# Optimization experiments

Hardware: AMD Instinct MI355X
Metric: run time of the kernel (lower is better)

## Reference

```python
import jax, jax.numpy as jnp
import numpy as np

# H2RConfig constants
KERNEL = 3
MAX_ROUTES = 1000
STRIDE = 4.0
MIN_SIZE = 32.0
MAX_SIZE = 512.0
SCORE_POWER = 2.0
UNC_WEIGHT = 0.35


def setup_inputs() -> dict:
    key = jax.random.key(0)
    k1, k2, k3 = jax.random.split(key, 3)
    shape = (32, 1, 512, 512)  # [B, 1, H, W] heatmaps at stride 4
    return {
        "route_logits": jax.random.normal(k1, shape, jnp.float32),
        "scale_logits": jax.random.normal(k2, shape, jnp.float32),
        "uncertainty_logits": jax.random.normal(k3, shape, jnp.float32),
        "image_h": 2048,
        "image_w": 2048,
    }


def reference(route_logits, scale_logits, uncertainty_logits, image_h, image_w):
    # score map: sigmoid^power, modulated by uncertainty (use_route_uncertainty=True)
    score = jnp.power(jax.nn.sigmoid(route_logits), SCORE_POWER)
    score = score * (1.0 - UNC_WEIGHT * jax.nn.sigmoid(uncertainty_logits))

    # local-max NMS: 3x3 max pool, stride 1, SAME padding (torch pads with -inf)
    pooled = jax.lax.reduce_window(
        score, -jnp.inf, jax.lax.max,
        window_dimensions=(1, 1, KERNEL, KERNEL),
        window_strides=(1, 1, 1, 1),
        padding="SAME",
    )
    peak_mask = score == pooled
    filtered = jnp.where(peak_mask, score, -1.0)

    B = score.shape[0]
    Wd = score.shape[3]
    flat = filtered.reshape(B, -1)                 # [B, H*W]
    values, indices = jax.lax.top_k(flat, MAX_ROUTES)  # [B, K]
    valid = values > 0.0                            # torch drops these; we mask/pad

    ys = indices // Wd
    xs = indices % Wd
    cx = (xs.astype(jnp.float32) + 0.5) * STRIDE
    cy = (ys.astype(jnp.float32) + 0.5) * STRIDE

    # gather scale / uncertainty at peak locations
    sc = jnp.take_along_axis(scale_logits.reshape(B, -1), indices, axis=1)
    un = jax.nn.sigmoid(jnp.take_along_axis(uncertainty_logits.reshape(B, -1), indices, axis=1))

    side = MIN_SIZE + jax.nn.sigmoid(sc) * (MAX_SIZE - MIN_SIZE)
    side = side * (1.0 + 0.25 * un)
    half = side * 0.5

    iw = float(image_w)
    ih = float(image_h)
    x1 = jnp.clip(cx - half, 0.0, iw - 1.0)
    y1 = jnp.clip(cy - half, 0.0, ih - 1.0)
    x2 = jnp.clip(cx + half, 1.0, iw)
    y2 = jnp.clip(cy + half, 1.0, ih)

    bcol = jnp.broadcast_to(jnp.arange(B, dtype=jnp.float32)[:, None], values.shape)
    rois = jnp.stack([bcol, x1, y1, x2, y2], axis=-1)  # [B, K, 5]

    # padded (fixed-shape) equivalent of torch's variable-length concat
    rois = jnp.where(valid[..., None], rois, 0.0)
    scores = jnp.where(valid, values, 0.0)
    return rois, scores, valid
```

## Files before the change

kernel.cpp:

```cpp
#include <hip/hip_runtime.h>
#include <hip/hip_bf16.h>
#include <math.h>


#define B_   32
#define H_   512
#define W_   512
#define HW_  (H_ * W_)
#define K_   1000
#define ROWS_ 16
#define THR_  512
#define NSTRIP_ 32
#define SEGCAP_ 1200
#define CAND_ 2048
#define NBUK_ 4096
#define NW_   (NBUK_ / 2)

__device__ __forceinline__ float np_expf(float x) {
#pragma clang fp contract(off)
    const float log2e = 1.44269504088896341f;
    float z = x * log2e;
    float m = rintf(z);
    float r = fmaf(m, -0.693359375f, x);
    r = fmaf(m, 2.12194440e-4f, r);
    float r2 = r * r;
    float p = fmaf(1.9875691500e-4f, r, 1.3981999507e-3f);
    p = fmaf(p, r, 8.3334519073e-3f);
    p = fmaf(p, r, 4.1665795894e-2f);
    p = fmaf(p, r, 1.6666665459e-1f);
    p = fmaf(p, r, 5.0000001201e-1f);
    p = fmaf(p, r2, r);
    p = p + 1.0f;
    int mi = (int)m;
    float sc = __int_as_float((127 + mi) << 23);
    return p * sc;
}

__device__ __forceinline__ float sigmoid_np(float x) {
#pragma clang fp contract(off)
    float e = np_expf(-x);
    float d = 1.0f + e;
    return 1.0f / d;
}

__device__ __forceinline__ float score_ref(float r, float u) {
#pragma clang fp contract(off)
    float s  = sigmoid_np(r);
    float s2 = s * s;
    float su = sigmoid_np(u);
    float t  = 0.35f * su;
    float m  = 1.0f - t;
    return s2 * m;
}

__device__ __forceinline__ float sigmoid_fast(float x) {
    return 1.0f / (1.0f + __expf(-x));
}

__global__ __launch_bounds__(THR_, 4) void fused_peak_kernel(
    const float* __restrict__ route, const float* __restrict__ unc,
    unsigned long long* __restrict__ plist, int* __restrict__ pcnt)
{
    __shared__ float sm[ROWS_ + 2][W_];
    __shared__ int lcnt;

    const int tid   = threadIdx.x;
    const int lane  = tid & 63;
    const int strip = blockIdx.x;
    const int b     = blockIdx.y;
    const int r0    = strip * ROWS_;
    if (tid == 0) lcnt = 0;

    const float4* rb4 = (const float4*)(route + (size_t)b * HW_);
    const float4* ub4 = (const float4*)(unc   + (size_t)b * HW_);
    unsigned long long* seg =
        plist + (size_t)(b * NSTRIP_ + strip) * SEGCAP_;

    float4 rv[5], uv[5];
    int lrow[5], c4[5]; bool ok[5];
    #pragma unroll
    for (int k = 0; k < 5; ++k) {
        int slot = tid + k * THR_;
        slot = slot < 2303 ? slot : 2303;
        int row = slot >> 7;
        int gy  = r0 - 1 + row;
        lrow[k] = row; c4[k] = slot & 127;
        ok[k]   = (gy >= 0 && gy < H_);
        int cy  = gy < 0 ? 0 : (gy >= H_ ? H_ - 1 : gy);
        rv[k] = rb4[cy * 128 + c4[k]];
        uv[k] = ub4[cy * 128 + c4[k]];
    }
    #pragma unroll
    for (int k = 0; k < 5; ++k) {
        float4 s;
        s.x = score_ref(rv[k].x, uv[k].x);
        s.y = score_ref(rv[k].y, uv[k].y);
        s.z = score_ref(rv[k].z, uv[k].z);
        s.w = score_ref(rv[k].w, uv[k].w);
        if (!ok[k]) { s.x = -INFINITY; s.y = -INFINITY;
                      s.z = -INFINITY; s.w = -INFINITY; }
        *(float4*)&sm[lrow[k]][c4[k] * 4] = s;
    }
    __syncthreads();

    #pragma unroll
    for (int j = 0; j < 4; ++j) {
        int g  = tid + j * THR_;
        int ly = 1 + (g >> 7);
        int x0 = (g & 127) * 4;
        int gy = r0 + (ly - 1);
        float4 q0 = *(const float4*)&sm[ly - 1][x0];
        float4 q1 = *(const float4*)&sm[ly    ][x0];
        float4 q2 = *(const float4*)&sm[ly + 1][x0];
        bool hasL = (x0 > 0), hasR = (x0 + 4 < W_);
        float l0 = hasL ? sm[ly - 1][x0 - 1] : -INFINITY;
        float l1 = hasL ? sm[ly    ][x0 - 1] : -INFINITY;
        float l2 = hasL ? sm[ly + 1][x0 - 1] : -INFINITY;
        float e0 = hasR ? sm[ly - 1][x0 + 4] : -INFINITY;
        float e1 = hasR ? sm[ly    ][x0 + 4] : -INFINITY;
        float e2 = hasR ? sm[ly + 1][x0 + 4] : -INFINITY;
        float f_m1 = fmaxf(l0, fmaxf(l1, l2));
        float f_0  = fmaxf(q0.x, fmaxf(q1.x, q2.x));
        float f_1  = fmaxf(q0.y, fmaxf(q1.y, q2.y));
        float f_2  = fmaxf(q0.z, fmaxf(q1.z, q2.z));
        float f_3  = fmaxf(q0.w, fmaxf(q1.w, q2.w));
        float f_4  = fmaxf(e0, fmaxf(e1, e2));
        float tb0  = fmaxf(q0.x, q2.x);
        float tb1  = fmaxf(q0.y, q2.y);
        float tb2  = fmaxf(q0.z, q2.z);
        float tb3  = fmaxf(q0.w, q2.w);
        float vv[4] = { q1.x, q1.y, q1.z, q1.w };
        float mm[4];
        mm[0] = fmaxf(fmaxf(f_m1, f_1), tb0);
        mm[1] = fmaxf(fmaxf(f_0,  f_2), tb1);
        mm[2] = fmaxf(fmaxf(f_1,  f_3), tb2);
        mm[3] = fmaxf(fmaxf(f_2,  f_4), tb3);
        #pragma unroll
        for (int i = 0; i < 4; ++i) {
            bool take = (vv[i] >= mm[i]);
            unsigned long long mk = __ballot(take);
            if (mk) {
                int ldr = __ffsll((unsigned long long)mk) - 1;
                int base_ = 0;
                if (lane == ldr) base_ = atomicAdd(&lcnt, __popcll(mk));
                base_ = __shfl(base_, ldr, 64);
                if (take) {
                    int p = base_ + __popcll(mk & ((1ull << lane) - 1ull));
                    unsigned int bits = __float_as_uint(vv[i]);
                    unsigned int idx  = (unsigned int)(gy * W_ + x0 + i);
                    if (p < SEGCAP_)
                        seg[p] = ((unsigned long long)bits << 32)
                                 | (0xFFFFFFFFu - idx);
                }
            }
        }
    }
    __syncthreads();
    if (tid == 0) {
        int n = lcnt < SEGCAP_ ? lcnt : SEGCAP_;
        pcnt[b * NSTRIP_ + strip] = n;
    }
}

__global__ __launch_bounds__(1024) void select_kernel(
    const float* __restrict__ scale, const float* __restrict__ unc,
    const unsigned long long* __restrict__ plist,
    const int* __restrict__ pcnt,
    const int* __restrict__ ih_p, const int* __restrict__ iw_p,
    float* __restrict__ out)
{
    __shared__ unsigned int h16[NW_];
    __shared__ unsigned long long cand[CAND_];
    __shared__ int scnt[NSTRIP_];
    __shared__ int sh_T, sh_n;

    const int b = blockIdx.x, tid = threadIdx.x;
    const int lane = tid & 63, wid = tid >> 6;
    if (tid == 0) { sh_T = 0; sh_n = 0; }
    if (tid < NSTRIP_) scnt[tid] = pcnt[b * NSTRIP_ + tid];
    for (int i = tid; i < NW_; i += 1024) h16[i] = 0u;
    __syncthreads();

    for (int s = 0; s < NSTRIP_; ++s) {
        int cnt = scnt[s];
        const unsigned long long* sg =
            plist + (size_t)(b * NSTRIP_ + s) * SEGCAP_;
        for (int i = tid; i < cnt; i += 1024) {
            unsigned int bkt = ((unsigned int)(sg[i] >> 32)) >> 18;
            atomicAdd(&h16[bkt >> 1], 1u << ((bkt & 1) * 16));
        }
    }
    __syncthreads();

    if (wid == 0) {
        int total = 0;
        for (int c = NBUK_ / 64 - 1; c >= 0; --c) {
            int bucket = c * 64 + lane;
            int cnt = (int)((h16[bucket >> 1] >> ((bucket & 1) * 16)) & 0xFFFFu);
            int sum = cnt;
            #pragma unroll
            for (int off = 32; off > 0; off >>= 1)
                sum += __shfl_down(sum, off, 64);
            sum = __shfl(sum, 0, 64);
            if (total + sum < K_) { total += sum; continue; }
            int suf = cnt;
            #pragma unroll
            for (int off = 1; off < 64; off <<= 1) {
                int o = __shfl_down(suf, off, 64);
                suf += (lane + off < 64) ? o : 0;
            }
            bool cond = (total + suf) >= K_;
            unsigned long long mask = __ballot(cond);
            int ls = 63 - __builtin_clzll(mask);
            if (lane == 0) sh_T = c * 64 + ls;
            break;
        }
    }
    __syncthreads();
    const unsigned int T = (unsigned int)sh_T;

    for (int s = 0; s < NSTRIP_; ++s) {
        int cnt = scnt[s];
        const unsigned long long* sg =
            plist + (size_t)(b * NSTRIP_ + s) * SEGCAP_;
        for (int i = tid; i < cnt; i += 1024) {
            unsigned long long key = sg[i];
            if (((((unsigned int)(key >> 32))) >> 18) >= T) {
                int p = atomicAdd(&sh_n, 1);
                if (p < CAND_) cand[p] = key;
            }
        }
    }
    __syncthreads();
    int nc = sh_n; if (nc > CAND_) nc = CAND_;
    int sortN = (nc <= 1024) ? 1024 : CAND_;
    for (int i = tid; i < sortN; i += 1024)
        if (i >= nc) cand[i] = 0ull;

    for (int kk = 2; kk <= sortN; kk <<= 1) {
        for (int jj = kk >> 1; jj > 0; jj >>= 1) {
            __syncthreads();
            for (int p = tid; p < (sortN >> 1); p += 1024) {
                int i   = ((p & ~(jj - 1)) << 1) | (p & (jj - 1));
                int ixj = i | jj;
                bool desc = ((i & kk) == 0);
                unsigned long long a = cand[i], c2 = cand[ixj];
                if (desc ? (a < c2) : (a > c2)) { cand[i] = c2; cand[ixj] = a; }
            }
        }
    }
    __syncthreads();

    const float fih = (float)(*ih_p);
    const float fiw = (float)(*iw_p);
    float* rois   = out;
    float* scores = out + (size_t)B_ * K_ * 5;
    float* validf = out + (size_t)B_ * K_ * 6;

    for (int k = tid; k < K_; k += 1024) {
        int o = b * K_ + k;
        unsigned long long key = cand[k];
        unsigned int bits = (unsigned int)(key >> 32);
        if (bits == 0u) {
            rois[o * 5 + 0] = 0.0f; rois[o * 5 + 1] = 0.0f;
            rois[o * 5 + 2] = 0.0f; rois[o * 5 + 3] = 0.0f;
            rois[o * 5 + 4] = 0.0f;
            scores[o] = 0.0f; validf[o] = 0.0f;
        } else {
            float v = __uint_as_float(bits);
            unsigned int idx = 0xFFFFFFFFu - (unsigned int)(key & 0xFFFFFFFFull);
            int y = (int)(idx >> 9), x = (int)(idx & 511u);
            float cx = ((float)x + 0.5f) * 4.0f;
            float cy = ((float)y + 0.5f) * 4.0f;
            float ss = sigmoid_fast(scale[(size_t)b * HW_ + idx]);
            float su = sigmoid_fast(unc  [(size_t)b * HW_ + idx]);
            float side = (32.0f + ss * 480.0f) * (1.0f + 0.25f * su);
            float half = 0.5f * side;
            float x1 = fminf(fmaxf(cx - half, 0.0f), fiw - 1.0f);
            float y1 = fminf(fmaxf(cy - half, 0.0f), fih - 1.0f);
            float x2 = fminf(fmaxf(cx + half, 1.0f), fiw);
            float y2 = fminf(fmaxf(cy + half, 1.0f), fih);
            rois[o * 5 + 0] = (float)b;
            rois[o * 5 + 1] = x1; rois[o * 5 + 2] = y1;
            rois[o * 5 + 3] = x2; rois[o * 5 + 4] = y2;
            scores[o] = v; validf[o] = 1.0f;
        }
    }
}

extern "C" void kernel_launch(void* const* d_in, const int* in_sizes, int n_in,
                              void* d_out, int out_size, void* d_ws, size_t ws_size,
                              hipStream_t stream) {
    const float* route = (const float*)d_in[0];
    const float* scale = (const float*)d_in[1];
    const float* unc   = (const float*)d_in[2];
    const int*   ih    = (const int*)d_in[3];
    const int*   iw    = (const int*)d_in[4];
    float* out = (float*)d_out;

    char* ws = (char*)d_ws;
    int* pcnt = (int*)ws;
    unsigned long long* plist = (unsigned long long*)(ws + 4096);

    dim3 g(NSTRIP_, B_);
    fused_peak_kernel<<<g, THR_, 0, stream>>>(route, unc, plist, pcnt);
    select_kernel<<<B_, 1024, 0, stream>>>(scale, unc, plist, pcnt,
                                           ih, iw, out);
}
```

Before: 174.5 us.

## Zero-pad peak segments and scan them with wide loads, sharded histograms, warp-aggregated appends

The peak kernel now zero-fills the unused tail of each strip segment instead of writing per-strip counts. The select kernel can then stream the whole per-batch slot array with 16-byte loads, unrolled two pairs deep, with no per-strip loop or count lookups. The histogram is split into four shared-memory copies to reduce atomic contention, and the candidate append uses one wave-aggregated atomic per ballot. In exchange, every padded slot is read (about 38K keys per batch, regardless of the real count) and the peak kernel spends extra stores writing zeros.

```diff
diff --git a/kernel.cpp b/kernel.cpp
--- a/kernel.cpp
+++ b/kernel.cpp
@@ -12,6 +12,8 @@
 #define THR_  512
 #define NSTRIP_ 32
 #define SEGCAP_ 1200
+#define NSLOT_ (NSTRIP_ * SEGCAP_)
+#define NPAIR_ (NSLOT_ / 2)
 #define CAND_ 2048
 #define NBUK_ 4096
 #define NW_   (NBUK_ / 2)
@@ -59,7 +61,7 @@
 
 __global__ __launch_bounds__(THR_, 4) void fused_peak_kernel(
     const float* __restrict__ route, const float* __restrict__ unc,
-    unsigned long long* __restrict__ plist, int* __restrict__ pcnt)
+    unsigned long long* __restrict__ plist)
 {
     __shared__ float sm[ROWS_ + 2][W_];
     __shared__ int lcnt;
@@ -156,47 +158,62 @@
         }
     }
     __syncthreads();
-    if (tid == 0) {
-        int n = lcnt < SEGCAP_ ? lcnt : SEGCAP_;
-        pcnt[b * NSTRIP_ + strip] = n;
-    }
+    int n = lcnt < SEGCAP_ ? lcnt : SEGCAP_;
+    for (int i = n + tid; i < SEGCAP_; i += THR_) seg[i] = 0ull;
 }
 
 __global__ __launch_bounds__(1024) void select_kernel(
     const float* __restrict__ scale, const float* __restrict__ unc,
     const unsigned long long* __restrict__ plist,
-    const int* __restrict__ pcnt,
     const int* __restrict__ ih_p, const int* __restrict__ iw_p,
     float* __restrict__ out)
 {
-    __shared__ unsigned int h16[NW_];
+    __shared__ unsigned int h4[4 * NW_];
     __shared__ unsigned long long cand[CAND_];
-    __shared__ int scnt[NSTRIP_];
     __shared__ int sh_T, sh_n;
 
     const int b = blockIdx.x, tid = threadIdx.x;
     const int lane = tid & 63, wid = tid >> 6;
     if (tid == 0) { sh_T = 0; sh_n = 0; }
-    if (tid < NSTRIP_) scnt[tid] = pcnt[b * NSTRIP_ + tid];
-    for (int i = tid; i < NW_; i += 1024) h16[i] = 0u;
-    __syncthreads();
-
-    for (int s = 0; s < NSTRIP_; ++s) {
-        int cnt = scnt[s];
-        const unsigned long long* sg =
-            plist + (size_t)(b * NSTRIP_ + s) * SEGCAP_;
-        for (int i = tid; i < cnt; i += 1024) {
-            unsigned int bkt = ((unsigned int)(sg[i] >> 32)) >> 18;
-            atomicAdd(&h16[bkt >> 1], 1u << ((bkt & 1) * 16));
-        }
-    }
+    for (int i = tid; i < 4 * NW_; i += 1024) h4[i] = 0u;
+    __syncthreads();
+
+    const ulonglong2* p2 =
+        (const ulonglong2*)(plist + (size_t)b * NSLOT_);
+    unsigned int* hw = h4 + (wid >> 2) * NW_;
+
+    {
+        int i = tid;
+        for (; i + 1024 < NPAIR_; i += 2048) {
+            ulonglong2 a = p2[i];
+            ulonglong2 c = p2[i + 1024];
+            unsigned int b0 = ((unsigned int)(a.x >> 32)) >> 18;
+            unsigned int b1 = ((unsigned int)(a.y >> 32)) >> 18;
+            unsigned int b2 = ((unsigned int)(c.x >> 32)) >> 18;
+            unsigned int b3 = ((unsigned int)(c.y >> 32)) >> 18;
+            if (b0) atomicAdd(&hw[b0 >> 1], 1u << ((b0 & 1) * 16));
+            if (b1) atomicAdd(&hw[b1 >> 1], 1u << ((b1 & 1) * 16));
+            if (b2) atomicAdd(&hw[b2 >> 1], 1u << ((b2 & 1) * 16));
+            if (b3) atomicAdd(&hw[b3 >> 1], 1u << ((b3 & 1) * 16));
+        }
+        for (; i < NPAIR_; i += 1024) {
+            ulonglong2 a = p2[i];
+            unsigned int b0 = ((unsigned int)(a.x >> 32)) >> 18;
+            unsigned int b1 = ((unsigned int)(a.y >> 32)) >> 18;
+            if (b0) atomicAdd(&hw[b0 >> 1], 1u << ((b0 & 1) * 16));
+            if (b1) atomicAdd(&hw[b1 >> 1], 1u << ((b1 & 1) * 16));
+        }
+    }
+    __syncthreads();
+    for (int i = tid; i < NW_; i += 1024)
+        h4[i] = h4[i] + h4[NW_ + i] + h4[2 * NW_ + i] + h4[3 * NW_ + i];
     __syncthreads();
 
     if (wid == 0) {
         int total = 0;
         for (int c = NBUK_ / 64 - 1; c >= 0; --c) {
             int bucket = c * 64 + lane;
-            int cnt = (int)((h16[bucket >> 1] >> ((bucket & 1) * 16)) & 0xFFFFu);
+            int cnt = (int)((h4[bucket >> 1] >> ((bucket & 1) * 16)) & 0xFFFFu);
             int sum = cnt;
             #pragma unroll
             for (int off = 32; off > 0; off >>= 1)
@@ -219,15 +236,45 @@
     __syncthreads();
     const unsigned int T = (unsigned int)sh_T;
 
-    for (int s = 0; s < NSTRIP_; ++s) {
-        int cnt = scnt[s];
-        const unsigned long long* sg =
-            plist + (size_t)(b * NSTRIP_ + s) * SEGCAP_;
-        for (int i = tid; i < cnt; i += 1024) {
-            unsigned long long key = sg[i];
-            if (((((unsigned int)(key >> 32))) >> 18) >= T) {
-                int p = atomicAdd(&sh_n, 1);
-                if (p < CAND_) cand[p] = key;
+    {
+        int i = tid;
+        for (; i + 1024 < NPAIR_; i += 2048) {
+            ulonglong2 a = p2[i];
+            ulonglong2 c = p2[i + 1024];
+            unsigned long long ks[4] = { a.x, a.y, c.x, c.y };
+            #pragma unroll
+            for (int q = 0; q < 4; ++q) {
+                bool take = ((((unsigned int)(ks[q] >> 32))) >> 18) >= T;
+                unsigned long long mk = __ballot(take);
+                if (mk) {
+                    int ldr = __ffsll((unsigned long long)mk) - 1;
+                    int base_ = 0;
+                    if (lane == ldr) base_ = atomicAdd(&sh_n, __popcll(mk));
+                    base_ = __shfl(base_, ldr, 64);
+                    if (take) {
+                        int p = base_ + __popcll(mk & ((1ull << lane) - 1ull));
+                        if (p < CAND_) cand[p] = ks[q];
+                    }
+                }
+            }
+        }
+        for (; i < NPAIR_; i += 1024) {
+            ulonglong2 a = p2[i];
+            unsigned long long ks[2] = { a.x, a.y };
+            #pragma unroll
+            for (int q = 0; q < 2; ++q) {
+                bool take = ((((unsigned int)(ks[q] >> 32))) >> 18) >= T;
+                unsigned long long mk = __ballot(take);
+                if (mk) {
+                    int ldr = __ffsll((unsigned long long)mk) - 1;
+                    int base_ = 0;
+                    if (lane == ldr) base_ = atomicAdd(&sh_n, __popcll(mk));
+                    base_ = __shfl(base_, ldr, 64);
+                    if (take) {
+                        int p = base_ + __popcll(mk & ((1ull << lane) - 1ull));
+                        if (p < CAND_) cand[p] = ks[q];
+                    }
+                }
             }
         }
     }
@@ -298,12 +345,9 @@
     const int*   iw    = (const int*)d_in[4];
     float* out = (float*)d_out;
 
-    char* ws = (char*)d_ws;
-    int* pcnt = (int*)ws;
-    unsigned long long* plist = (unsigned long long*)(ws + 4096);
+    unsigned long long* plist = (unsigned long long*)d_ws;
 
     dim3 g(NSTRIP_, B_);
-    fused_peak_kernel<<<g, THR_, 0, stream>>>(route, unc, plist, pcnt);
-    select_kernel<<<B_, 1024, 0, stream>>>(scale, unc, plist, pcnt,
-                                           ih, iw, out);
-}
+    fused_peak_kernel<<<g, THR_, 0, stream>>>(route, unc, plist);
+    select_kernel<<<B_, 1024, 0, stream>>>(scale, unc, plist, ih, iw, out);
+}
```

Result: faster. 163.4 us (-6.4%).

## Pre-bucket peaks by score class per strip to skip select-kernel histogram pass

Applied to the files above, without the earlier changes.

The peak kernel now stages peaks in shared memory, builds a 512-class histogram over the score's float-bit exponent and mantissa bits, and writes each strip's peaks to global memory grouped by class, with the per-class counts emitted as 16-bit values. The select kernel sums these per-strip histograms to find the threshold class, then copies whole class-prefix ranges straight into the candidate buffer. This removes the select kernel's global histogram atomics and its filtered compaction pass. In exchange it adds shared-memory use and extra passes in the peak kernel, which may lower occupancy, and the candidate set (up to 4096) can be coarser, giving a larger bitonic sort.

```diff
diff --git a/kernel.cpp b/kernel.cpp
--- a/kernel.cpp
+++ b/kernel.cpp
@@ -12,9 +12,13 @@
 #define THR_  512
 #define NSTRIP_ 32
 #define SEGCAP_ 1200
-#define CAND_ 2048
-#define NBUK_ 4096
-#define NW_   (NBUK_ / 2)
+#define NCLS_ 512
+#define CAND4_ 4096
+
+__device__ __forceinline__ int class_of(unsigned int bits) {
+    int cls = 2031 - (int)(bits >> 19);
+    return cls > (NCLS_ - 1) ? (NCLS_ - 1) : cls;
+}
 
 __device__ __forceinline__ float np_expf(float x) {
 #pragma clang fp contract(off)
@@ -59,17 +63,22 @@
 
 __global__ __launch_bounds__(THR_, 4) void fused_peak_kernel(
     const float* __restrict__ route, const float* __restrict__ unc,
-    unsigned long long* __restrict__ plist, int* __restrict__ pcnt)
+    unsigned long long* __restrict__ plist, unsigned short* __restrict__ cnt16)
 {
     __shared__ float sm[ROWS_ + 2][W_];
+    __shared__ unsigned long long pbuf[SEGCAP_];
+    __shared__ unsigned int ccnt[NCLS_];
+    __shared__ unsigned int coff[NCLS_];
     __shared__ int lcnt;
 
     const int tid   = threadIdx.x;
     const int lane  = tid & 63;
+    const int wid   = tid >> 6;
     const int strip = blockIdx.x;
     const int b     = blockIdx.y;
     const int r0    = strip * ROWS_;
     if (tid == 0) lcnt = 0;
+    if (tid < NCLS_) ccnt[tid] = 0u;
 
     const float4* rb4 = (const float4*)(route + (size_t)b * HW_);
     const float4* ub4 = (const float4*)(unc   + (size_t)b * HW_);
@@ -149,93 +158,132 @@
                     unsigned int bits = __float_as_uint(vv[i]);
                     unsigned int idx  = (unsigned int)(gy * W_ + x0 + i);
                     if (p < SEGCAP_)
-                        seg[p] = ((unsigned long long)bits << 32)
-                                 | (0xFFFFFFFFu - idx);
+                        pbuf[p] = ((unsigned long long)bits << 32)
+                                  | (0xFFFFFFFFu - idx);
                 }
             }
         }
     }
     __syncthreads();
-    if (tid == 0) {
-        int n = lcnt < SEGCAP_ ? lcnt : SEGCAP_;
-        pcnt[b * NSTRIP_ + strip] = n;
-    }
+    const int n = lcnt < SEGCAP_ ? lcnt : SEGCAP_;
+
+    for (int i = tid; i < n; i += THR_)
+        atomicAdd(&ccnt[class_of((unsigned int)(pbuf[i] >> 32))], 1u);
+    __syncthreads();
+
+    if (wid == 0) {
+        int carry = 0;
+        for (int k = 0; k < NCLS_ / 64; ++k) {
+            int c = k * 64 + lane;
+            int v = (int)ccnt[c];
+            int pre = v;
+            #pragma unroll
+            for (int off = 1; off < 64; off <<= 1) {
+                int o = __shfl_up(pre, off, 64);
+                if (lane >= off) pre += o;
+            }
+            coff[c] = (unsigned int)(carry + pre - v);
+            carry += __shfl(pre, 63, 64);
+        }
+    }
+    __syncthreads();
+
+    for (int i = tid; i < n; i += THR_) {
+        unsigned long long key = pbuf[i];
+        int cls = class_of((unsigned int)(key >> 32));
+        unsigned int pos = atomicAdd(&coff[cls], 1u);
+        seg[pos] = key;
+    }
+    if (tid < NCLS_)
+        cnt16[(size_t)(b * NSTRIP_ + strip) * NCLS_ + tid] =
+            (unsigned short)ccnt[tid];
 }
 
 __global__ __launch_bounds__(1024) void select_kernel(
     const float* __restrict__ scale, const float* __restrict__ unc,
     const unsigned long long* __restrict__ plist,
-    const int* __restrict__ pcnt,
+    const unsigned short* __restrict__ cnt16,
     const int* __restrict__ ih_p, const int* __restrict__ iw_p,
     float* __restrict__ out)
 {
-    __shared__ unsigned int h16[NW_];
-    __shared__ unsigned long long cand[CAND_];
-    __shared__ int scnt[NSTRIP_];
-    __shared__ int sh_T, sh_n;
+    __shared__ __align__(16) unsigned char smem[CAND4_ * 8];
+    __shared__ unsigned int tot[NCLS_];
+    __shared__ int slen[NSTRIP_], sbase[NSTRIP_];
+    __shared__ int sh_C, sh_n;
+
+    unsigned int* scnt = (unsigned int*)smem;
+    unsigned long long* cand = (unsigned long long*)smem;
 
     const int b = blockIdx.x, tid = threadIdx.x;
     const int lane = tid & 63, wid = tid >> 6;
-    if (tid == 0) { sh_T = 0; sh_n = 0; }
-    if (tid < NSTRIP_) scnt[tid] = pcnt[b * NSTRIP_ + tid];
-    for (int i = tid; i < NW_; i += 1024) h16[i] = 0u;
-    __syncthreads();
-
+    if (tid == 0) { sh_C = NCLS_ - 1; sh_n = 0; }
+
+    const unsigned int* g =
+        (const unsigned int*)(cnt16 + (size_t)b * NSTRIP_ * NCLS_);
+    for (int i = tid; i < NSTRIP_ * NCLS_ / 2; i += 1024) scnt[i] = g[i];
+    __syncthreads();
+
+    if (tid < NCLS_) {
+        unsigned int s = 0;
+        for (int st = 0; st < NSTRIP_; ++st) {
+            unsigned int w = scnt[st * (NCLS_ / 2) + (tid >> 1)];
+            s += (tid & 1) ? (w >> 16) : (w & 0xFFFFu);
+        }
+        tot[tid] = s;
+    }
+    __syncthreads();
+
+    if (wid == 0) {
+        int cum = 0;
+        for (int k = 0; k < NCLS_ / 64; ++k) {
+            int c = k * 64 + lane;
+            int v = (int)tot[c];
+            int pre = v;
+            #pragma unroll
+            for (int off = 1; off < 64; off <<= 1) {
+                int o = __shfl_up(pre, off, 64);
+                if (lane >= off) pre += o;
+            }
+            int ctot = __shfl(pre, 63, 64);
+            if (cum + ctot < K_) { cum += ctot; continue; }
+            bool cond = (cum + pre) >= K_;
+            unsigned long long mask = __ballot(cond);
+            int fs = __ffsll((unsigned long long)mask) - 1;
+            if (lane == 0) sh_C = k * 64 + fs;
+            break;
+        }
+    }
+    __syncthreads();
+    const int Cstar = sh_C;
+
+    if (tid < NSTRIP_) {
+        int len = 0;
+        for (int c = 0; c <= Cstar; ++c) {
+            unsigned int w = scnt[tid * (NCLS_ / 2) + (c >> 1)];
+            len += (c & 1) ? (int)(w >> 16) : (int)(w & 0xFFFFu);
+        }
+        slen[tid] = len;
+    }
+    __syncthreads();
+    if (tid == 0) {
+        int acc = 0;
+        for (int s = 0; s < NSTRIP_; ++s) { sbase[s] = acc; acc += slen[s]; }
+        sh_n = acc;
+    }
+    __syncthreads();
+
+    const int n = sh_n < CAND4_ ? sh_n : CAND4_;
     for (int s = 0; s < NSTRIP_; ++s) {
-        int cnt = scnt[s];
+        int len = slen[s], base = sbase[s];
         const unsigned long long* sg =
             plist + (size_t)(b * NSTRIP_ + s) * SEGCAP_;
-        for (int i = tid; i < cnt; i += 1024) {
-            unsigned int bkt = ((unsigned int)(sg[i] >> 32)) >> 18;
-            atomicAdd(&h16[bkt >> 1], 1u << ((bkt & 1) * 16));
-        }
-    }
-    __syncthreads();
-
-    if (wid == 0) {
-        int total = 0;
-        for (int c = NBUK_ / 64 - 1; c >= 0; --c) {
-            int bucket = c * 64 + lane;
-            int cnt = (int)((h16[bucket >> 1] >> ((bucket & 1) * 16)) & 0xFFFFu);
-            int sum = cnt;
-            #pragma unroll
-            for (int off = 32; off > 0; off >>= 1)
-                sum += __shfl_down(sum, off, 64);
-            sum = __shfl(sum, 0, 64);
-            if (total + sum < K_) { total += sum; continue; }
-            int suf = cnt;
-            #pragma unroll
-            for (int off = 1; off < 64; off <<= 1) {
-                int o = __shfl_down(suf, off, 64);
-                suf += (lane + off < 64) ? o : 0;
-            }
-            bool cond = (total + suf) >= K_;
-            unsigned long long mask = __ballot(cond);
-            int ls = 63 - __builtin_clzll(mask);
-            if (lane == 0) sh_T = c * 64 + ls;
-            break;
-        }
-    }
-    __syncthreads();
-    const unsigned int T = (unsigned int)sh_T;
-
-    for (int s = 0; s < NSTRIP_; ++s) {
-        int cnt = scnt[s];
-        const unsigned long long* sg =
-            plist + (size_t)(b * NSTRIP_ + s) * SEGCAP_;
-        for (int i = tid; i < cnt; i += 1024) {
-            unsigned long long key = sg[i];
-            if (((((unsigned int)(key >> 32))) >> 18) >= T) {
-                int p = atomicAdd(&sh_n, 1);
-                if (p < CAND_) cand[p] = key;
-            }
-        }
-    }
-    __syncthreads();
-    int nc = sh_n; if (nc > CAND_) nc = CAND_;
-    int sortN = (nc <= 1024) ? 1024 : CAND_;
+        for (int i = tid; i < len; i += 1024)
+            if (base + i < CAND4_) cand[base + i] = sg[i];
+    }
+    __syncthreads();
+    int sortN = (n <= 1024) ? 1024 : ((n <= 2048) ? 2048 : CAND4_);
     for (int i = tid; i < sortN; i += 1024)
-        if (i >= nc) cand[i] = 0ull;
+        if (i >= n) cand[i] = 0ull;
 
     for (int kk = 2; kk <= sortN; kk <<= 1) {
         for (int jj = kk >> 1; jj > 0; jj >>= 1) {
@@ -298,12 +346,12 @@
     const int*   iw    = (const int*)d_in[4];
     float* out = (float*)d_out;
 
-    char* ws = (char*)d_ws;
-    int* pcnt = (int*)ws;
-    unsigned long long* plist = (unsigned long long*)(ws + 4096);
+    unsigned short* cnt16 = (unsigned short*)d_ws;
+    unsigned long long* plist =
+        (unsigned long long*)((char*)d_ws + (size_t)B_ * NSTRIP_ * NCLS_ * 2);
 
     dim3 g(NSTRIP_, B_);
-    fused_peak_kernel<<<g, THR_, 0, stream>>>(route, unc, plist, pcnt);
-    select_kernel<<<B_, 1024, 0, stream>>>(scale, unc, plist, pcnt,
+    fused_peak_kernel<<<g, THR_, 0, stream>>>(route, unc, plist, cnt16);
+    select_kernel<<<B_, 1024, 0, stream>>>(scale, unc, plist, cnt16,
                                            ih, iw, out);
 }
```

After: 170.4 us. -2.4%, faster.
